# Performance work log

Hardware: AMD Instinct MI355X
Metric: run time of the kernel (lower is better)

Reference implementation:

```python
import jax, jax.numpy as jnp
import numpy as np

N_HEADS, N_KV, HEAD_DIM = 16, 4, 64
DIM = 4096
LATENT = N_HEADS * HEAD_DIM   # 1024
KV_DIM = N_KV * HEAD_DIM      # 256
KSZ = 3


def _causal_conv1d(x, w, b, groups):
    # x: [B,S,C]; w: [Cout, Cin//groups, K]; causal left padding (K-1)
    y = jax.lax.conv_general_dilated(
        x.transpose(0, 2, 1), w, window_strides=(1,),
        padding=[(w.shape[-1] - 1, 0)], feature_group_count=groups,
        dimension_numbers=('NCH', 'OIH', 'NCH'))
    return (y + b[None, :, None]).transpose(0, 2, 1)


def _rope(x, cos, sin):
    # x: [B,H,S,D] interleaved pairs; cos/sin: [1,1,S,D//2]
    x1, x2 = x[..., ::2], x[..., 1::2]
    out = jnp.stack([x1 * cos - x2 * sin, x1 * sin + x2 * cos], axis=-1)
    return out.reshape(x.shape)


def _l2norm(x):
    n = jnp.sqrt(jnp.sum(x * x, axis=-1, keepdims=True))
    return x / jnp.maximum(n, 1e-12)


def setup_inputs() -> dict:
    key = jax.random.key(0)
    ks = jax.random.split(key, 12)
    sc = 0.02
    x = jax.random.normal(ks[0], (2, 2048, DIM), jnp.float32)
    w_qkv = jax.random.normal(ks[1], (LATENT + 2 * KV_DIM, DIM), jnp.float32) * sc
    w_o = jax.random.normal(ks[2], (DIM, LATENT), jnp.float32) * sc
    qc1_w = jax.random.normal(ks[3], (LATENT, LATENT // N_HEADS, KSZ), jnp.float32) * sc
    qc1_b = jnp.zeros((LATENT,), jnp.float32)
    qc2_w = jax.random.normal(ks[4], (LATENT, LATENT, KSZ), jnp.float32) * sc
    qc2_b = jnp.zeros((LATENT,), jnp.float32)
    kc1_w = jax.random.normal(ks[5], (KV_DIM, KV_DIM // N_KV, KSZ), jnp.float32) * sc
    kc1_b = jnp.zeros((KV_DIM,), jnp.float32)
    kc2_w = jax.random.normal(ks[6], (KV_DIM, KV_DIM, KSZ), jnp.float32) * sc
    kc2_b = jnp.zeros((KV_DIM,), jnp.float32)
    key_temp = jnp.full((1,), float(HEAD_DIM) ** 0.5, jnp.float32)
    return dict(x=x, w_qkv=w_qkv, w_o=w_o, qc1_w=qc1_w, qc1_b=qc1_b,
                qc2_w=qc2_w, qc2_b=qc2_b, kc1_w=kc1_w, kc1_b=kc1_b,
                kc2_w=kc2_w, kc2_b=kc2_b, key_temp=key_temp)


def _forward(x, w_qkv, w_o, qc1_w, qc1_b, qc2_w, qc2_b, kc1_w, kc1_b, kc2_w, kc2_b, key_temp):
    B, S, _ = x.shape
    qkv = x @ w_qkv.T  # [B,S,LATENT+2*KV_DIM]
    q = qkv[..., :LATENT]
    k = qkv[..., LATENT:LATENT + KV_DIM]
    # value shift: first half current token, second half previous token (0 at t=0)
    half = KV_DIM // 2
    v_curr = qkv[..., LATENT + KV_DIM:LATENT + KV_DIM + half]
    v_prev = qkv[..., LATENT + KV_DIM + half:]
    v = jnp.concatenate([v_curr, jnp.pad(v_prev[:, :-1, :], ((0, 0), (1, 0), (0, 0)))], axis=-1)
    q_pre, k_pre = q, k
    # grouped causal conv sequences on q and k
    q = _causal_conv1d(_causal_conv1d(q, qc1_w, qc1_b, N_HEADS), qc2_w, qc2_b, 1)
    k = _causal_conv1d(_causal_conv1d(k, kc1_w, kc1_b, N_KV), kc2_w, kc2_b, 1)
    # qk-mean coupling (n_groups = 4 branch)
    q_mean = q_pre.reshape(B, S, N_HEADS, HEAD_DIM).mean(axis=2)  # [B,S,hd]
    k_mean = k_pre.reshape(B, S, N_KV, HEAD_DIM).mean(axis=2)
    q = q.reshape(B, S, N_HEADS, HEAD_DIM) + 0.5 * k_mean[:, :, None, :]
    k = k.reshape(B, S, N_KV, HEAD_DIM) + 0.5 * q_mean[:, :, None, :]
    q = q.transpose(0, 2, 1, 3)                                   # [B,H,S,d]
    k = k.transpose(0, 2, 1, 3)                                   # [B,Hkv,S,d]
    v = v.reshape(B, S, N_KV, HEAD_DIM).transpose(0, 2, 1, 3)
    # qk-norm with learned key temperature
    q = _l2norm(q)
    k = _l2norm(k) * key_temp
    # RoPE (interleaved pairs)
    inv = 1.0 / (10000.0 ** (jnp.arange(0, HEAD_DIM, 2, dtype=jnp.float32) / HEAD_DIM))
    ang = jnp.arange(S, dtype=jnp.float32)[:, None] * inv[None, :]  # [S,d/2]
    cos, sin = jnp.cos(ang)[None, None], jnp.sin(ang)[None, None]
    q = _rope(q, cos, sin)
    k = _rope(k, cos, sin)
    # GQA: each kv head repeated n_groups times contiguously
    kg = jnp.repeat(k, N_HEADS // N_KV, axis=1)
    vg = jnp.repeat(v, N_HEADS // N_KV, axis=1)
    scale = HEAD_DIM ** -0.5
    scores = jnp.einsum('bhqd,bhkd->bhqk', q, kg) * scale
    causal = jnp.tril(jnp.ones((S, S), dtype=bool))
    scores = jnp.where(causal[None, None], scores, jnp.finfo(scores.dtype).min)
    attn = jax.nn.softmax(scores, axis=-1)
    out = jnp.einsum('bhqk,bhkd->bhqd', attn, vg)
    out = out.transpose(0, 2, 1, 3).reshape(B, S, LATENT)
    return out @ w_o.T  # output_scale = 1.0


def reference(x, w_qkv, w_o, qc1_w, qc1_b, qc2_w, qc2_b, kc1_w, kc1_b, kc2_w, kc2_b, key_temp):
    return _forward(x, w_qkv, w_o, qc1_w, qc1_b, qc2_w, qc2_b, kc1_w, kc1_b, kc2_w, kc2_b, key_temp)
```

## Files before the change

### kernel.cpp

```cpp
#include <hip/hip_runtime.h>
#include <hip/hip_bf16.h>
#include <cstddef>

#define NB 2
#define SEQ 2048
#define DIMX 4096
#define NH 16
#define NKV 4
#define HD 64
#define LATENT 1024
#define KVD 256
#define QKVN 1536
#define BS (NB*SEQ)
#define SP (SEQ+2)

typedef __attribute__((ext_vector_type(8))) short short8v;
typedef __attribute__((ext_vector_type(4))) float f32x4;
typedef __attribute__((ext_vector_type(4))) unsigned short ushort4v;
typedef __attribute__((ext_vector_type(4))) unsigned int uint4v;

static __device__ __forceinline__ unsigned short f2bf(float f) {
    union { float f; unsigned u; } v; v.f = f;
    unsigned r = v.u + 0x7fffu + ((v.u >> 16) & 1u);
    return (unsigned short)(r >> 16);
}

static __device__ __forceinline__ unsigned cvt_pk_bf16(float lo, float hi) {
    unsigned r;
    asm("v_cvt_pk_bf16_f32 %0, %1, %2" : "=v"(r) : "v"(lo), "v"(hi));
    return r;
}

static __device__ __forceinline__ void gload_lds16(const unsigned short* g, unsigned short* l) {
    __builtin_amdgcn_global_load_lds((const __attribute__((address_space(1))) void*)g,
                                     (__attribute__((address_space(3))) void*)l, 16, 0, 0);
}

#define XC_BLK (BS*DIMX/4/256)
#define WC_BLK (QKVN*DIMX/4/256)
__global__ __launch_bounds__(256)
void cast_inputs(const float* __restrict__ x, unsigned short* __restrict__ xb,
                 const float* __restrict__ wq, unsigned short* __restrict__ wqb)
{
    const int blk = blockIdx.x;
    const float* in; unsigned short* out; int i;
    if (blk < XC_BLK) { in = x; out = xb; i = blk * 256 + threadIdx.x; }
    else              { in = wq; out = wqb; i = (blk - XC_BLK) * 256 + threadIdx.x; }
    const float4 v = *reinterpret_cast<const float4*>(in + (size_t)i * 4);
    ushort4v o = {f2bf(v.x), f2bf(v.y), f2bf(v.z), f2bf(v.w)};
    *reinterpret_cast<ushort4v*>(out + (size_t)i * 4) = o;
}

#define WO_BLK 4096
#define QW_N (LATENT*LATENT*3)
#define QW_BLK 12288
#define KW_N (KVD*KVD*3)
#define KW_BLK 768
#define RT_BLK 256
__global__ __launch_bounds__(256)
void prep_misc(const float* __restrict__ wo, unsigned short* __restrict__ wob,
               const float* __restrict__ qc2w, unsigned short* __restrict__ qc2wr,
               const float* __restrict__ kc2w, unsigned short* __restrict__ kc2wr,
               float2* __restrict__ rtab,
               unsigned short* __restrict__ pq, unsigned short* __restrict__ pk)
{
    const int blk = blockIdx.x, tid = threadIdx.x;
    if (blk < WO_BLK) {
        const int i = blk * 256 + tid;
        const float4 v = *reinterpret_cast<const float4*>(wo + (size_t)i * 4);
        ushort4v o = {f2bf(v.x), f2bf(v.y), f2bf(v.z), f2bf(v.w)};
        *reinterpret_cast<ushort4v*>(wob + (size_t)i * 4) = o;
    } else if (blk < WO_BLK + QW_BLK) {
        const int idx = (blk - WO_BLK) * 256 + tid;
        if (idx < QW_N) {
            const int o = idx / (LATENT * 3), rem = idx % (LATENT * 3);
            const int j = rem / LATENT, c = rem % LATENT;
            qc2wr[idx] = f2bf(qc2w[(size_t)o * LATENT * 3 + c * 3 + j]);
        }
    } else if (blk < WO_BLK + QW_BLK + KW_BLK) {
        const int idx = (blk - WO_BLK - QW_BLK) * 256 + tid;
        if (idx < KW_N) {
            const int o = idx / (KVD * 3), rem = idx % (KVD * 3);
            const int j = rem / KVD, c = rem % KVD;
            kc2wr[idx] = f2bf(kc2w[(size_t)o * KVD * 3 + c * 3 + j]);
        }
    } else if (blk < WO_BLK + QW_BLK + KW_BLK + RT_BLK) {
        const int idx = (blk - WO_BLK - QW_BLK - KW_BLK) * 256 + tid;
        const int s = idx >> 5, i = idx & 31;
        const float inv = powf(10000.f, -(float)(2 * i) * (1.f / HD));
        const float ang = (float)s * inv;
        rtab[idx] = make_float2(cosf(ang), sinf(ang));
    } else {
        const int t = (blk - WO_BLK - QW_BLK - KW_BLK - RT_BLK) * 256 + tid;
        if (t < 2 * 2 * LATENT) {
            const int b = t / (2 * LATENT), r = (t % (2 * LATENT)) / LATENT, c = t % LATENT;
            pq[((size_t)b * SP + r) * LATENT + c] = 0;
        }
        if (t < 2 * 2 * KVD) {
            const int b = t / (2 * KVD), r = (t % (2 * KVD)) / KVD, c = t % KVD;
            pk[((size_t)b * SP + r) * KVD + c] = 0;
        }
    }
}

template<int CONV>
__global__ __launch_bounds__(256)
void gemm_bf16(const unsigned short* __restrict__ A, const unsigned short* __restrict__ W,
               const float* __restrict__ bias, float* __restrict__ C,
               int M, int N, int K, int Cch, int klen, size_t ps1, size_t ps2)
{
    __shared__ unsigned short Abuf[2][128 * 32];
    __shared__ unsigned short Bbuf[2][128 * 32];
    const int gx = gridDim.x;
    const int nwg = gx * gridDim.y;
    const int lin = blockIdx.y * gx + blockIdx.x;
    const int swz = (lin & 7) * (nwg >> 3) + (lin >> 3);
    const int n0 = (swz % gx) * 128, m0 = (swz / gx) * 128;
    const int koff = blockIdx.z * klen;
    C += (blockIdx.z == 1) ? ps1 : (blockIdx.z == 2 ? ps2 : 0);
    const int tid = threadIdx.x;
    const int wave = tid >> 6, lane = tid & 63;
    const int lg = lane >> 4, lr = lane & 15;
    const int wm = (wave & 1) * 64, wn = (wave >> 1) * 64;
    const int sr = wave * 32 + (lane >> 2);
    const int sc = (lane & 3) * 8;
    const int bb = m0 / SEQ, s0 = m0 % SEQ;

    const int NT = klen / 32;
    f32x4 acc[4][4];
    #pragma unroll
    for (int i = 0; i < 4; i++)
        #pragma unroll
        for (int j = 0; j < 4; j++) acc[i][j] = (f32x4){0.f, 0.f, 0.f, 0.f};

    auto stage = [&](int buf, int kt) {
        const int k0 = koff + kt * 32;
        const unsigned short* ga0;
        if (!CONV) {
            ga0 = A + (size_t)(m0 + sr) * K + k0 + sc;
        } else {
            const int j = k0 / Cch, c0 = k0 - j * Cch;
            ga0 = A + (size_t)(bb * SP + s0 + j + sr) * Cch + c0 + sc;
        }
        const unsigned short* gb0 = W + (size_t)(n0 + sr) * K + k0 + sc;
        const size_t astep = (size_t)16 * (CONV ? Cch : K);
        #pragma unroll
        for (int i = 0; i < 2; i++) {
            gload_lds16(ga0 + i * astep, &Abuf[buf][(wave * 2 + i) * 512]);
            gload_lds16(gb0 + (size_t)i * 16 * K, &Bbuf[buf][(wave * 2 + i) * 512]);
        }
    };

    stage(0, 0);
    __syncthreads();
    int cur = 0;
    for (int kt = 0; kt < NT; ++kt) {
        if (kt + 1 < NT) stage(cur ^ 1, kt + 1);
        short8v af[4], bf[4];
        #pragma unroll
        for (int mi = 0; mi < 4; mi++)
            af[mi] = *reinterpret_cast<const short8v*>(&Abuf[cur][(wm + mi * 16 + lr) * 32 + lg * 8]);
        #pragma unroll
        for (int ni = 0; ni < 4; ni++)
            bf[ni] = *reinterpret_cast<const short8v*>(&Bbuf[cur][(wn + ni * 16 + lr) * 32 + lg * 8]);
        #pragma unroll
        for (int mi = 0; mi < 4; mi++)
            #pragma unroll
            for (int ni = 0; ni < 4; ni++)
                acc[mi][ni] = __builtin_amdgcn_mfma_f32_16x16x32_bf16(af[mi], bf[ni], acc[mi][ni], 0, 0, 0);
        __syncthreads();
        cur ^= 1;
    }

    #pragma unroll
    for (int ni = 0; ni < 4; ni++) {
        const int col = n0 + wn + ni * 16 + lr;
        const float bv = bias ? bias[col] : 0.f;
        #pragma unroll
        for (int mi = 0; mi < 4; mi++)
            #pragma unroll
            for (int r = 0; r < 4; r++)
                C[(size_t)(m0 + wm + mi * 16 + lg * 4 + r) * N + col] = acc[mi][ni][r] + bv;
    }
}

__global__ __launch_bounds__(256)
void conv1_grouped(const float* __restrict__ qkv0, const float* __restrict__ qkv1,
                   const float* __restrict__ qw, const float* __restrict__ qb,
                   const float* __restrict__ kw, const float* __restrict__ kb,
                   unsigned short* __restrict__ pq, unsigned short* __restrict__ pk)
{
    const int t0 = blockIdx.x * 64;
    const int b  = blockIdx.y;
    const int z  = blockIdx.z;
    const bool isq = (z < NH);
    const int g  = isq ? z : z - NH;
    const int coloff = isq ? 0 : LATENT;
    const float* w = isq ? qw : kw;
    const float* bias = isq ? qb : kb;
    unsigned short* out = isq ? pq : pk;
    const int CH = isq ? LATENT : KVD;

    __shared__ float xs[66][64];
    for (int idx = threadIdx.x; idx < 66 * 64; idx += 256) {
        const int i = idx >> 6, ic = idx & 63;
        const int tt = t0 + i - 2;
        float v = 0.f;
        if (tt >= 0) {
            const size_t off = (size_t)(b * SEQ + tt) * QKVN + coloff + g * 64 + ic;
            v = qkv0[off] + qkv1[off];
        }
        xs[i][ic] = v;
    }
    __syncthreads();
    const int oc = threadIdx.x & 63;
    const int ibase = (threadIdx.x >> 6) * 16;
    float acc[16];
    const float bv = bias[g * 64 + oc];
    #pragma unroll
    for (int i = 0; i < 16; i++) acc[i] = bv;
    const float* wp = w + (size_t)(g * 64 + oc) * 192;
    for (int ic = 0; ic < 64; ic++) {
        const float w0 = wp[ic * 3 + 0], w1 = wp[ic * 3 + 1], w2 = wp[ic * 3 + 2];
        float xv[18];
        #pragma unroll
        for (int r = 0; r < 18; r++) xv[r] = xs[ibase + r][ic];
        #pragma unroll
        for (int i = 0; i < 16; i++) acc[i] += w0 * xv[i] + w1 * xv[i + 1] + w2 * xv[i + 2];
    }
    #pragma unroll
    for (int i = 0; i < 16; i++)
        out[((size_t)b * SP + 2 + t0 + ibase + i) * CH + g * 64 + oc] = f2bf(acc[i]);
}

__global__ __launch_bounds__(64)
void meanv_kernel(const float* __restrict__ qkv0, const float* __restrict__ qkv1,
                  float* __restrict__ qmean, float* __restrict__ kmean,
                  unsigned short* __restrict__ vRow)
{
    const int t = blockIdx.x, d = threadIdx.x;
    const int b = t >> 11, s = t & (SEQ - 1);
    const float* r0 = qkv0 + (size_t)t * QKVN;
    const float* r1 = qkv1 + (size_t)t * QKVN;
    float qs = 0.f;
    #pragma unroll
    for (int h = 0; h < NH; h++) qs += r0[h * 64 + d] + r1[h * 64 + d];
    qmean[t * 64 + d] = qs * (1.f / NH);
    float ks = 0.f;
    #pragma unroll
    for (int h = 0; h < NKV; h++) ks += r0[LATENT + h * 64 + d] + r1[LATENT + h * 64 + d];
    kmean[t * 64 + d] = ks * (1.f / NKV);
    #pragma unroll
    for (int g = 0; g < NKV; g++) {
        const int c = g * 64 + d;
        float v;
        if (c < 128) {
            v = r0[LATENT + KVD + c] + r1[LATENT + KVD + c];
        } else {
            v = 0.f;
            if (s > 0) {
                const size_t off = (size_t)(t - 1) * QKVN + LATENT + KVD + 128 + (c - 128);
                v = qkv0[off] + qkv1[off];
            }
        }
        vRow[((size_t)(b * NKV + g) * SEQ + s) * 64 + d] = f2bf(v);
    }
}

__global__ __launch_bounds__(256)
void vtrans(const unsigned short* __restrict__ vRow, unsigned short* __restrict__ vTb)
{
    const int s0 = blockIdx.x * 64;
    const int bg = blockIdx.y;
    __shared__ unsigned short t[64][72];
    const int tid = threadIdx.x;
    {
        const int r = tid >> 2, c0 = (tid & 3) * 16;
        const unsigned short* p = vRow + ((size_t)bg * SEQ + s0 + r) * 64 + c0;
        const short8v a = *reinterpret_cast<const short8v*>(p);
        const short8v bv = *reinterpret_cast<const short8v*>(p + 8);
        #pragma unroll
        for (int j = 0; j < 8; j++) { t[r][c0 + j] = (unsigned short)a[j]; t[r][c0 + 8 + j] = (unsigned short)bv[j]; }
    }
    __syncthreads();
    {
        const int d = tid >> 2, ss = (tid & 3) * 16;
        short8v o0, o1;
        #pragma unroll
        for (int j = 0; j < 8; j++) { o0[j] = (short)t[ss + j][d]; o1[j] = (short)t[ss + 8 + j][d]; }
        unsigned short* op = vTb + ((size_t)bg * 64 + d) * SEQ + s0 + ss;
        *reinterpret_cast<short8v*>(op) = o0;
        *reinterpret_cast<short8v*>(op + 8) = o1;
    }
}

__global__ __launch_bounds__(64)
void qk_final(const float* __restrict__ qc2a, const float* __restrict__ qc2b, const float* __restrict__ qc2c,
              const float* __restrict__ kc2a, const float* __restrict__ kc2b,
              const float* __restrict__ qbias, const float* __restrict__ kbias,
              const float* __restrict__ qmean, const float* __restrict__ kmean,
              const float* __restrict__ key_temp, const float2* __restrict__ rtab,
              unsigned short* __restrict__ qTb, unsigned short* __restrict__ kTb)
{
    const int t = blockIdx.x, hh = blockIdx.y, d = threadIdx.x;
    const int b = t >> 11, s = t & (SEQ - 1);
    float val;
    if (hh < NH) {
        const size_t off = (size_t)t * LATENT + hh * 64 + d;
        val = qc2a[off] + qc2b[off] + qc2c[off] + qbias[hh * 64 + d] + 0.5f * kmean[t * 64 + d];
    } else {
        const size_t off = (size_t)t * KVD + (hh - NH) * 64 + d;
        val = kc2a[off] + kc2b[off] + kbias[(hh - NH) * 64 + d] + 0.5f * qmean[t * 64 + d];
    }
    float ss = val * val;
    #pragma unroll
    for (int off = 32; off >= 1; off >>= 1) ss += __shfl_xor(ss, off);
    const float n = sqrtf(ss);
    val = val / fmaxf(n, 1e-12f);
    if (hh >= NH) val *= key_temp[0];
    const float2 cs = rtab[s * 32 + (d >> 1)];
    const float cv = cs.x, sv = cs.y;
    const float partner = __shfl_xor(val, 1);
    const float x1 = (d & 1) ? partner : val;
    const float x2 = (d & 1) ? val : partner;
    const float o = (d & 1) ? (x1 * sv + x2 * cv) : (x1 * cv - x2 * sv);
    if (hh < NH) qTb[((size_t)(b * NH + hh) * SEQ + s) * 64 + d] = f2bf(o);
    else         kTb[((size_t)(b * NKV + (hh - NH)) * SEQ + s) * 64 + d] = f2bf(o);
}

__global__ __launch_bounds__(256)
void attn_mfma(const unsigned short* __restrict__ qTb, const unsigned short* __restrict__ kTb,
               const unsigned short* __restrict__ vTb,
               unsigned short* __restrict__ pnum, float* __restrict__ pden)
{
    const int wg = blockIdx.x;
    const int qg = wg >> 8;
    const int u = wg & 255;
    const int xcd = u & 7, i = u >> 3;
    const int bh = (xcd << 2) | (i >> 3);
    const int r = i & 7;
    const int p = (qg == 0) ? r : (qg == 1) ? (15 - r) : (qg == 2) ? (16 + r) : (31 - r);
    const int blk = 15 - (p >> 1);
    const int part = p & 1;
    const int half = blk + 1;
    const int cbeg = part * half, cend = cbeg + half;

    const int b = bh >> 4, h = bh & 15, g = h >> 2;
    const int tid = threadIdx.x;
    const int wave = tid >> 6, lane = tid & 63;
    const int lg = lane >> 4, lr = lane & 15;
    const int qt = blk * 4 + wave;
    const int q0 = qt * 32;

    __shared__ __align__(16) unsigned short SB[2][16][512];

    short8v qf[2][2];
    const unsigned short* qbase = qTb + ((size_t)(b * NH + h) * SEQ + q0) * 64;
    #pragma unroll
    for (int mf = 0; mf < 2; mf++)
        #pragma unroll
        for (int dc = 0; dc < 2; dc++)
            qf[mf][dc] = *reinterpret_cast<const short8v*>(qbase + (size_t)(mf * 16 + lr) * 64 + dc * 32 + lg * 8);

    f32x4 acc[2][4];
    float lsum[2] = {0.f, 0.f};
    #pragma unroll
    for (int mf = 0; mf < 2; mf++)
        #pragma unroll
        for (int dt = 0; dt < 4; dt++) acc[mf][dt] = (f32x4){0.f, 0.f, 0.f, 0.f};

    const unsigned short* kbase = kTb + (size_t)(b * NKV + g) * SEQ * 64;
    const unsigned short* vbase = vTb + (size_t)(b * NKV + g) * 64 * SEQ;
    const float EC = 0.125f * 1.44269504f;
    const int src01 = ((lg & 1) << 5) + lr;
    const int src23 = src01 + 16;
    const bool hi = (lg >= 2);

    auto stage64 = [&](int buf, int cc) {
        const int kb = cc * 64;
        #pragma unroll
        for (int i2 = 0; i2 < 4; i2++) {
            const int ch = wave * 4 + i2;
            const int st = ch >> 3, chl = ch & 7;
            const int k0 = kb + st * 32;
            const unsigned short* src;
            if (chl < 4) src = kbase + (size_t)(k0 + (chl >> 1) * 16 + lr) * 64 + (chl & 1) * 32 + lg * 8;
            else         src = vbase + (size_t)((chl - 4) * 16 + lr) * SEQ + k0 + lg * 8;
            gload_lds16(src, &SB[buf][ch][lane * 8]);
        }
    };

    stage64(0, cbeg);
    __syncthreads();
    int cur = 0;
    for (int cc = cbeg; cc < cend; ++cc) {
        if (cc + 1 < cend) stage64(cur ^ 1, cc + 1);
        #pragma unroll
        for (int st = 0; st < 2; ++st) {
            const int c = cc * 2 + st;
            if (c > qt) continue;
            const int k0 = c * 32;
            short8v kf[2][2], vf[4];
            #pragma unroll
            for (int kt = 0; kt < 2; kt++)
                #pragma unroll
                for (int dc = 0; dc < 2; dc++)
                    kf[kt][dc] = *reinterpret_cast<const short8v*>(&SB[cur][st * 8 + kt * 2 + dc][lane * 8]);
            #pragma unroll
            for (int dt = 0; dt < 4; dt++)
                vf[dt] = *reinterpret_cast<const short8v*>(&SB[cur][st * 8 + 4 + dt][lane * 8]);

            const bool diag = (c == qt);
            #pragma unroll
            for (int mf = 0; mf < 2; mf++) {
                f32x4 z0 = (f32x4){0.f, 0.f, 0.f, 0.f}, z1 = (f32x4){0.f, 0.f, 0.f, 0.f};
                __builtin_amdgcn_s_setprio(1);
                z0 = __builtin_amdgcn_mfma_f32_16x16x32_bf16(kf[0][0], qf[mf][0], z0, 0, 0, 0);
                z0 = __builtin_amdgcn_mfma_f32_16x16x32_bf16(kf[0][1], qf[mf][1], z0, 0, 0, 0);
                z1 = __builtin_amdgcn_mfma_f32_16x16x32_bf16(kf[1][0], qf[mf][0], z1, 0, 0, 0);
                z1 = __builtin_amdgcn_mfma_f32_16x16x32_bf16(kf[1][1], qf[mf][1], z1, 0, 0, 0);
                __builtin_amdgcn_s_setprio(0);
                float p0[4], p1[4];
                #pragma unroll
                for (int rr = 0; rr < 4; rr++) {
                    p0[rr] = exp2f(z0[rr] * EC);
                    p1[rr] = exp2f(z1[rr] * EC);
                }
                if (diag) {
                    const int q = q0 + mf * 16 + lr;
                    #pragma unroll
                    for (int rr = 0; rr < 4; rr++) {
                        if (k0 + 4 * lg + rr > q)      p0[rr] = 0.f;
                        if (k0 + 16 + 4 * lg + rr > q) p1[rr] = 0.f;
                    }
                }
                lsum[mf] += (p0[0] + p0[1]) + (p0[2] + p0[3]) + (p1[0] + p1[1]) + (p1[2] + p1[3]);
                const unsigned W00 = cvt_pk_bf16(p0[0], p0[1]);
                const unsigned W01 = cvt_pk_bf16(p0[2], p0[3]);
                const unsigned W10 = cvt_pk_bf16(p1[0], p1[1]);
                const unsigned W11 = cvt_pk_bf16(p1[2], p1[3]);
                const unsigned a0 = __shfl(W00, src01), b0 = __shfl(W10, src01);
                const unsigned a1 = __shfl(W01, src01), b1 = __shfl(W11, src01);
                const unsigned a2 = __shfl(W00, src23), b2 = __shfl(W10, src23);
                const unsigned a3 = __shfl(W01, src23), b3 = __shfl(W11, src23);
                uint4v pw;
                pw.x = hi ? b0 : a0;
                pw.y = hi ? b1 : a1;
                pw.z = hi ? b2 : a2;
                pw.w = hi ? b3 : a3;
                const short8v pa = __builtin_bit_cast(short8v, pw);
                __builtin_amdgcn_s_setprio(1);
                #pragma unroll
                for (int dt = 0; dt < 4; dt++)
                    acc[mf][dt] = __builtin_amdgcn_mfma_f32_16x16x32_bf16(pa, vf[dt], acc[mf][dt], 0, 0, 0);
                __builtin_amdgcn_s_setprio(0);
            }
        }
        __syncthreads();
        cur ^= 1;
    }

    float den[2];
    #pragma unroll
    for (int mf = 0; mf < 2; mf++) {
        float s = lsum[mf];
        s += __shfl_xor(s, 16); s += __shfl_xor(s, 32);
        den[mf] = s;
    }

    const int base = ((bh * 64 + qt) * 2 + part);
    if (lg == 0) {
        pden[base * 32 + lr] = den[0];
        pden[base * 32 + 16 + lr] = den[1];
    }
    unsigned short* np = pnum + (size_t)base * 2048;
    #pragma unroll
    for (int mf = 0; mf < 2; mf++)
        #pragma unroll
        for (int dt = 0; dt < 4; dt++)
            #pragma unroll
            for (int rr = 0; rr < 4; rr++)
                np[(mf * 16 + 4 * lg + rr) * 64 + dt * 16 + lr] = f2bf(acc[mf][dt][rr]);
}

__global__ __launch_bounds__(256)
void attn_merge(const unsigned short* __restrict__ pnum, const float* __restrict__ pden,
                unsigned short* __restrict__ attnb)
{
    const int idx = blockIdx.x * 256 + threadIdx.x;
    const int d0 = (idx & 7) * 8;
    const int qr = (idx >> 3) & 31;
    const int qt = (idx >> 8) & 63;
    const int bh = idx >> 14;
    const int base = (bh * 64 + qt) * 2;
    const float den = pden[base * 32 + qr] + pden[(base + 1) * 32 + qr];
    const float inv = 1.f / den;
    const short8v n0 = *reinterpret_cast<const short8v*>(pnum + (size_t)base * 2048 + qr * 64 + d0);
    const short8v n1 = *reinterpret_cast<const short8v*>(pnum + (size_t)(base + 1) * 2048 + qr * 64 + d0);
    short8v ov;
    #pragma unroll
    for (int j = 0; j < 8; j++) {
        union { unsigned u; float f; } t0, t1;
        t0.u = ((unsigned)(unsigned short)n0[j]) << 16;
        t1.u = ((unsigned)(unsigned short)n1[j]) << 16;
        ov[j] = (short)f2bf((t0.f + t1.f) * inv);
    }
    const int q = qt * 32 + qr;
    const int b = bh >> 4, h = bh & 15;
    *reinterpret_cast<short8v*>(attnb + (size_t)(b * SEQ + q) * LATENT + h * 64 + d0) = ov;
}

extern "C" void kernel_launch(void* const* d_in, const int* in_sizes, int n_in,
                              void* d_out, int out_size, void* d_ws, size_t ws_size,
                              hipStream_t stream)
{
    const float* x       = (const float*)d_in[0];
    const float* w_qkv   = (const float*)d_in[1];
    const float* w_o     = (const float*)d_in[2];
    const float* qc1_w   = (const float*)d_in[3];
    const float* qc1_b   = (const float*)d_in[4];
    const float* qc2_w   = (const float*)d_in[5];
    const float* qc2_b   = (const float*)d_in[6];
    const float* kc1_w   = (const float*)d_in[7];
    const float* kc1_b   = (const float*)d_in[8];
    const float* kc2_w   = (const float*)d_in[9];
    const float* kc2_b   = (const float*)d_in[10];
    const float* key_temp = (const float*)d_in[11];

    char* wsb = (char*)d_ws;
    float* qkv = (float*)wsb;                 wsb += (size_t)BS * QKVN * 4;
    float* qc2 = qkv;
    float* kc2 = (float*)((char*)qkv + (size_t)BS * LATENT * 4);
    unsigned short* pq  = (unsigned short*)wsb;  wsb += (size_t)NB * SP * LATENT * 2;
    unsigned short* pk  = (unsigned short*)wsb;  wsb += (size_t)NB * SP * KVD * 2;
    float* qmean = (float*)wsb;  wsb += (size_t)BS * HD * 4;
    float* kmean = (float*)wsb;  wsb += (size_t)BS * HD * 4;
    unsigned short* qTb  = (unsigned short*)wsb;  wsb += (size_t)BS * LATENT * 2;
    unsigned short* kTb  = (unsigned short*)wsb;  wsb += (size_t)BS * KVD * 2;
    unsigned short* vRow = (unsigned short*)wsb;  wsb += (size_t)BS * KVD * 2;
    unsigned short* vTb  = (unsigned short*)wsb;  wsb += (size_t)BS * KVD * 2;
    unsigned short* xb   = (unsigned short*)wsb;  wsb += (size_t)BS * DIMX * 2;
    unsigned short* attnb  = xb;
    unsigned short* qc2wr  = (unsigned short*)((char*)xb + (size_t)BS * LATENT * 2);
    unsigned short* kc2wr  = (unsigned short*)((char*)qc2wr + (size_t)LATENT * LATENT * 3 * 2);
    unsigned short* wqkvb = (unsigned short*)wsb;  wsb += (size_t)QKVN * DIMX * 2;
    unsigned short* wob   = wqkvb;

    float* outp = (float*)d_out;

    float* qkvp1 = outp;
    const size_t QKV_PS = (size_t)((ptrdiff_t)(qkvp1 - qkv));
    float* qc2p1 = (float*)((char*)d_ws + 67512320);
    float* qc2p2 = outp;
    const size_t QC2_PS1 = (size_t)(qc2p1 - qc2);
    const size_t QC2_PS2 = (size_t)((ptrdiff_t)(qc2p2 - qc2));
    float* kc2p1 = (float*)((char*)d_ws + (size_t)BS * QKVN * 4);
    const size_t KC2_PS1 = (size_t)(kc2p1 - kc2);
    float2* rtab = (float2*)((char*)d_ws + 84289536);
    unsigned short* apnum = (unsigned short*)d_ws;
    float* apden = (float*)((char*)d_ws + 16777216);

    cast_inputs<<<dim3(XC_BLK + WC_BLK), 256, 0, stream>>>(x, xb, w_qkv, wqkvb);
    gemm_bf16<0><<<dim3(QKVN / 128, BS / 128, 2), 256, 0, stream>>>(xb, wqkvb, nullptr, qkv, BS, QKVN, DIMX, 0, DIMX / 2, QKV_PS, 0);
    prep_misc<<<dim3(WO_BLK + QW_BLK + KW_BLK + RT_BLK + 16), 256, 0, stream>>>(
        w_o, wob, qc2_w, qc2wr, kc2_w, kc2wr, rtab, pq, pk);
    meanv_kernel<<<dim3(BS), 64, 0, stream>>>(qkv, qkvp1, qmean, kmean, vRow);
    vtrans<<<dim3(SEQ / 64, NB * NKV), 256, 0, stream>>>(vRow, vTb);
    conv1_grouped<<<dim3(SEQ / 64, NB, NH + NKV), 256, 0, stream>>>(qkv, qkvp1, qc1_w, qc1_b, kc1_w, kc1_b, pq, pk);
    gemm_bf16<1><<<dim3(LATENT / 128, BS / 128, 3), 256, 0, stream>>>(pq, qc2wr, nullptr, qc2, BS, LATENT, LATENT * 3, LATENT, LATENT, QC2_PS1, QC2_PS2);
    gemm_bf16<1><<<dim3(KVD / 128, BS / 128, 2), 256, 0, stream>>>(pk, kc2wr, nullptr, kc2, BS, KVD, KVD * 3, KVD, KVD * 3 / 2, KC2_PS1, 0);
    qk_final<<<dim3(BS, NH + NKV), 64, 0, stream>>>(qc2, qc2p1, qc2p2, kc2, kc2p1, qc2_b, kc2_b,
                                                    qmean, kmean, key_temp, rtab, qTb, kTb);
    attn_mfma<<<dim3(1024), 256, 0, stream>>>(qTb, kTb, vTb, apnum, apden);
    attn_merge<<<dim3(2048), 256, 0, stream>>>(apnum, apden, attnb);
    gemm_bf16<0><<<dim3(DIMX / 128, BS / 128, 1), 256, 0, stream>>>(attnb, wob, nullptr, outp, BS, DIMX, LATENT, 0, LATENT, 0, 0);
}
```

Baseline: 338.5 us.

## Fuse mean/V-shift with V transpose, widen qk_final blocks, MFMA softmax denominators

The separate meanv and vtrans kernels become one kernel that builds the shifted V tile in shared memory and writes the transposed layout directly, removing the vRow round trip and one launch. qk_final now processes four tokens per 256-thread block instead of one token per 64-thread block, to cut block scheduling overhead. In attention, the softmax row sums now come from an extra MFMA against a vector of bf16 ones instead of scalar adds plus shuffles. That sums the bf16-rounded probabilities, which matches the numerator more closely, but adds one MFMA per step.

```diff
diff --git a/kernel.cpp b/kernel.cpp
--- a/kernel.cpp
+++ b/kernel.cpp
@@ -233,68 +233,59 @@
         out[((size_t)b * SP + 2 + t0 + ibase + i) * CH + g * 64 + oc] = f2bf(acc[i]);
 }
 
-__global__ __launch_bounds__(64)
-void meanv_kernel(const float* __restrict__ qkv0, const float* __restrict__ qkv1,
+__global__ __launch_bounds__(256)
+void meanv_vtrans(const float* __restrict__ qkv0, const float* __restrict__ qkv1,
                   float* __restrict__ qmean, float* __restrict__ kmean,
-                  unsigned short* __restrict__ vRow)
-{
-    const int t = blockIdx.x, d = threadIdx.x;
-    const int b = t >> 11, s = t & (SEQ - 1);
-    const float* r0 = qkv0 + (size_t)t * QKVN;
-    const float* r1 = qkv1 + (size_t)t * QKVN;
-    float qs = 0.f;
-    #pragma unroll
-    for (int h = 0; h < NH; h++) qs += r0[h * 64 + d] + r1[h * 64 + d];
-    qmean[t * 64 + d] = qs * (1.f / NH);
-    float ks = 0.f;
-    #pragma unroll
-    for (int h = 0; h < NKV; h++) ks += r0[LATENT + h * 64 + d] + r1[LATENT + h * 64 + d];
-    kmean[t * 64 + d] = ks * (1.f / NKV);
-    #pragma unroll
-    for (int g = 0; g < NKV; g++) {
-        const int c = g * 64 + d;
-        float v;
-        if (c < 128) {
-            v = r0[LATENT + KVD + c] + r1[LATENT + KVD + c];
-        } else {
-            v = 0.f;
-            if (s > 0) {
-                const size_t off = (size_t)(t - 1) * QKVN + LATENT + KVD + 128 + (c - 128);
-                v = qkv0[off] + qkv1[off];
+                  unsigned short* __restrict__ vTb)
+{
+    const int s0 = blockIdx.x * 16;
+    const int b  = blockIdx.y;
+    const int tid = threadIdx.x;
+    const int w = tid >> 6, d = tid & 63;
+    __shared__ unsigned short vt[4][16][72];
+
+    #pragma unroll
+    for (int i = 0; i < 4; i++) {
+        const int s = s0 + w * 4 + i;
+        const int t = b * SEQ + s;
+        const float* r0 = qkv0 + (size_t)t * QKVN;
+        const float* r1 = qkv1 + (size_t)t * QKVN;
+        float qs = 0.f;
+        #pragma unroll
+        for (int h = 0; h < NH; h++) qs += r0[h * 64 + d] + r1[h * 64 + d];
+        qmean[(size_t)t * 64 + d] = qs * (1.f / NH);
+        float ks = 0.f;
+        #pragma unroll
+        for (int h = 0; h < NKV; h++) ks += r0[LATENT + h * 64 + d] + r1[LATENT + h * 64 + d];
+        kmean[(size_t)t * 64 + d] = ks * (1.f / NKV);
+        #pragma unroll
+        for (int g = 0; g < 4; g++) {
+            float v;
+            if (g < 2) {
+                v = r0[LATENT + KVD + g * 64 + d] + r1[LATENT + KVD + g * 64 + d];
+            } else {
+                v = 0.f;
+                if (s > 0) {
+                    const size_t off = (size_t)(t - 1) * QKVN + LATENT + KVD + 128 + (g - 2) * 64 + d;
+                    v = qkv0[off] + qkv1[off];
+                }
             }
-        }
-        vRow[((size_t)(b * NKV + g) * SEQ + s) * 64 + d] = f2bf(v);
-    }
-}
-
-__global__ __launch_bounds__(256)
-void vtrans(const unsigned short* __restrict__ vRow, unsigned short* __restrict__ vTb)
-{
-    const int s0 = blockIdx.x * 64;
-    const int bg = blockIdx.y;
-    __shared__ unsigned short t[64][72];
-    const int tid = threadIdx.x;
-    {
-        const int r = tid >> 2, c0 = (tid & 3) * 16;
-        const unsigned short* p = vRow + ((size_t)bg * SEQ + s0 + r) * 64 + c0;
-        const short8v a = *reinterpret_cast<const short8v*>(p);
-        const short8v bv = *reinterpret_cast<const short8v*>(p + 8);
-        #pragma unroll
-        for (int j = 0; j < 8; j++) { t[r][c0 + j] = (unsigned short)a[j]; t[r][c0 + 8 + j] = (unsigned short)bv[j]; }
+            vt[g][w * 4 + i][d] = f2bf(v);
+        }
     }
     __syncthreads();
     {
-        const int d = tid >> 2, ss = (tid & 3) * 16;
+        const int g = tid >> 6, dd = tid & 63;
         short8v o0, o1;
         #pragma unroll
-        for (int j = 0; j < 8; j++) { o0[j] = (short)t[ss + j][d]; o1[j] = (short)t[ss + 8 + j][d]; }
-        unsigned short* op = vTb + ((size_t)bg * 64 + d) * SEQ + s0 + ss;
+        for (int j = 0; j < 8; j++) { o0[j] = (short)vt[g][j][dd]; o1[j] = (short)vt[g][8 + j][dd]; }
+        unsigned short* op = vTb + ((size_t)(b * NKV + g) * 64 + dd) * SEQ + s0;
         *reinterpret_cast<short8v*>(op) = o0;
         *reinterpret_cast<short8v*>(op + 8) = o1;
     }
 }
 
-__global__ __launch_bounds__(64)
+__global__ __launch_bounds__(256)
 void qk_final(const float* __restrict__ qc2a, const float* __restrict__ qc2b, const float* __restrict__ qc2c,
               const float* __restrict__ kc2a, const float* __restrict__ kc2b,
               const float* __restrict__ qbias, const float* __restrict__ kbias,
@@ -302,7 +293,9 @@
               const float* __restrict__ key_temp, const float2* __restrict__ rtab,
               unsigned short* __restrict__ qTb, unsigned short* __restrict__ kTb)
 {
-    const int t = blockIdx.x, hh = blockIdx.y, d = threadIdx.x;
+    const int t = blockIdx.x * 4 + (threadIdx.x >> 6);
+    const int hh = blockIdx.y;
+    const int d = threadIdx.x & 63;
     const int b = t >> 11, s = t & (SEQ - 1);
     float val;
     if (hh < NH) {
@@ -362,12 +355,18 @@
         for (int dc = 0; dc < 2; dc++)
             qf[mf][dc] = *reinterpret_cast<const short8v*>(qbase + (size_t)(mf * 16 + lr) * 64 + dc * 32 + lg * 8);
 
+    short8v onesf;
+    #pragma unroll
+    for (int j = 0; j < 8; j++) onesf[j] = (short)0x3F80;
+
     f32x4 acc[2][4];
-    float lsum[2] = {0.f, 0.f};
-    #pragma unroll
-    for (int mf = 0; mf < 2; mf++)
+    f32x4 accden[2];
+    #pragma unroll
+    for (int mf = 0; mf < 2; mf++) {
+        accden[mf] = (f32x4){0.f, 0.f, 0.f, 0.f};
         #pragma unroll
         for (int dt = 0; dt < 4; dt++) acc[mf][dt] = (f32x4){0.f, 0.f, 0.f, 0.f};
+    }
 
     const unsigned short* kbase = kTb + (size_t)(b * NKV + g) * SEQ * 64;
     const unsigned short* vbase = vTb + (size_t)(b * NKV + g) * 64 * SEQ;
@@ -434,7 +433,6 @@
                         if (k0 + 16 + 4 * lg + rr > q) p1[rr] = 0.f;
                     }
                 }
-                lsum[mf] += (p0[0] + p0[1]) + (p0[2] + p0[3]) + (p1[0] + p1[1]) + (p1[2] + p1[3]);
                 const unsigned W00 = cvt_pk_bf16(p0[0], p0[1]);
                 const unsigned W01 = cvt_pk_bf16(p0[2], p0[3]);
                 const unsigned W10 = cvt_pk_bf16(p1[0], p1[1]);
@@ -453,6 +451,7 @@
                 #pragma unroll
                 for (int dt = 0; dt < 4; dt++)
                     acc[mf][dt] = __builtin_amdgcn_mfma_f32_16x16x32_bf16(pa, vf[dt], acc[mf][dt], 0, 0, 0);
+                accden[mf] = __builtin_amdgcn_mfma_f32_16x16x32_bf16(pa, onesf, accden[mf], 0, 0, 0);
                 __builtin_amdgcn_s_setprio(0);
             }
         }
@@ -460,18 +459,13 @@
         cur ^= 1;
     }
 
-    float den[2];
-    #pragma unroll
-    for (int mf = 0; mf < 2; mf++) {
-        float s = lsum[mf];
-        s += __shfl_xor(s, 16); s += __shfl_xor(s, 32);
-        den[mf] = s;
-    }
-
     const int base = ((bh * 64 + qt) * 2 + part);
-    if (lg == 0) {
-        pden[base * 32 + lr] = den[0];
-        pden[base * 32 + 16 + lr] = den[1];
+    if (lr == 0) {
+        #pragma unroll
+        for (int mf = 0; mf < 2; mf++)
+            #pragma unroll
+            for (int rr = 0; rr < 4; rr++)
+                pden[base * 32 + mf * 16 + 4 * lg + rr] = accden[mf][rr];
     }
     unsigned short* np = pnum + (size_t)base * 2048;
     #pragma unroll
@@ -545,6 +539,7 @@
     unsigned short* kc2wr  = (unsigned short*)((char*)qc2wr + (size_t)LATENT * LATENT * 3 * 2);
     unsigned short* wqkvb = (unsigned short*)wsb;  wsb += (size_t)QKVN * DIMX * 2;
     unsigned short* wob   = wqkvb;
+    (void)vRow;
 
     float* outp = (float*)d_out;
 
@@ -564,13 +559,12 @@
     gemm_bf16<0><<<dim3(QKVN / 128, BS / 128, 2), 256, 0, stream>>>(xb, wqkvb, nullptr, qkv, BS, QKVN, DIMX, 0, DIMX / 2, QKV_PS, 0);
     prep_misc<<<dim3(WO_BLK + QW_BLK + KW_BLK + RT_BLK + 16), 256, 0, stream>>>(
         w_o, wob, qc2_w, qc2wr, kc2_w, kc2wr, rtab, pq, pk);
-    meanv_kernel<<<dim3(BS), 64, 0, stream>>>(qkv, qkvp1, qmean, kmean, vRow);
-    vtrans<<<dim3(SEQ / 64, NB * NKV), 256, 0, stream>>>(vRow, vTb);
+    meanv_vtrans<<<dim3(SEQ / 16, NB), 256, 0, stream>>>(qkv, qkvp1, qmean, kmean, vTb);
     conv1_grouped<<<dim3(SEQ / 64, NB, NH + NKV), 256, 0, stream>>>(qkv, qkvp1, qc1_w, qc1_b, kc1_w, kc1_b, pq, pk);
     gemm_bf16<1><<<dim3(LATENT / 128, BS / 128, 3), 256, 0, stream>>>(pq, qc2wr, nullptr, qc2, BS, LATENT, LATENT * 3, LATENT, LATENT, QC2_PS1, QC2_PS2);
     gemm_bf16<1><<<dim3(KVD / 128, BS / 128, 2), 256, 0, stream>>>(pk, kc2wr, nullptr, kc2, BS, KVD, KVD * 3, KVD, KVD * 3 / 2, KC2_PS1, 0);
-    qk_final<<<dim3(BS, NH + NKV), 64, 0, stream>>>(qc2, qc2p1, qc2p2, kc2, kc2p1, qc2_b, kc2_b,
-                                                    qmean, kmean, key_temp, rtab, qTb, kTb);
+    qk_final<<<dim3(BS / 4, NH + NKV), 256, 0, stream>>>(qc2, qc2p1, qc2p2, kc2, kc2p1, qc2_b, kc2_b,
+                                                         qmean, kmean, key_temp, rtab, qTb, kTb);
     attn_mfma<<<dim3(1024), 256, 0, stream>>>(qTb, kTb, vTb, apnum, apden);
     attn_merge<<<dim3(2048), 256, 0, stream>>>(apnum, apden, attnb);
     gemm_bf16<0><<<dim3(DIMX / 128, BS / 128, 1), 256, 0, stream>>>(attnb, wob, nullptr, outp, BS, DIMX, LATENT, 0, LATENT, 0, 0);
```

New measurement: 339.0 us, median of 2. About the same (+0.1%).
